# Kernel optimization log

Hardware: AMD Instinct MI355X
Metric: run time of the kernel (lower is better)

The kernel has to match this reference:

```python
import jax, jax.numpy as jnp
import numpy as np

H = 4096      # hidden_size
NH = 32       # num heads
HD = H // NH  # head_dim = 128
I = 11008     # intermediate_size
T = 1024      # prompt tokens
G = 128       # AWQ group size
EPS = 1e-6
ROPE_BASE = 10000.0


def _pack4(key, in_f, out_f):
    # pack 8 uint4 nibbles per int32, [in_f, out_f/8]
    nib = jax.random.randint(key, (in_f, out_f // 8, 8), 0, 16, dtype=jnp.int32)
    shifts = (jnp.arange(8, dtype=jnp.int32) * 4)
    return jnp.bitwise_or.reduce(nib << shifts, axis=-1).astype(jnp.int32)


def _dequant(qw, qz, sc):
    # qw:[in,out/8] int32, qz:[in/G,out/8] int32, sc:[in/G,out] float
    shifts = jnp.arange(8, dtype=jnp.int32) * 4
    w = ((qw[:, :, None] >> shifts) & 0xF).reshape(qw.shape[0], -1)   # [in,out]
    z = ((qz[:, :, None] >> shifts) & 0xF).reshape(qz.shape[0], -1)   # [groups,out]
    gidx = jnp.arange(qw.shape[0]) // G
    return (w.astype(sc.dtype) - z.astype(sc.dtype)[gidx]) * sc[gidx]


def _qlinear(x, qw, qz, sc):
    return x @ _dequant(qw, qz, sc)


def _rmsnorm(x, w):
    var = jnp.mean(x * x, axis=-1, keepdims=True)
    return x * jax.lax.rsqrt(var + EPS) * w


def _rope(x, positions):
    # x: [T, NH, HD], neox-style half rotation (vLLM rotary)
    inv = 1.0 / (ROPE_BASE ** (jnp.arange(0, HD, 2, dtype=jnp.float32) / HD))
    freqs = positions.astype(jnp.float32)[:, None] * inv[None, :]     # [T, HD/2]
    cos = jnp.cos(freqs)[:, None, :]
    sin = jnp.sin(freqs)[:, None, :]
    x1, x2 = jnp.split(x, 2, axis=-1)
    return jnp.concatenate([x1 * cos - x2 * sin, x2 * cos + x1 * sin], axis=-1)


def _attention(positions, q, k, v):
    # causal self-attention over the prompt (prefill writes k/v to cache then attends)
    q = _rope(q.reshape(T, NH, HD), positions)
    k = _rope(k.reshape(T, NH, HD), positions)
    v = v.reshape(T, NH, HD)
    scale = HD ** -0.5
    scores = jnp.einsum('qhd,khd->hqk', q, k) * scale
    mask = jnp.tril(jnp.ones((T, T), dtype=bool))
    scores = jnp.where(mask[None], scores, jnp.finfo(scores.dtype).min)
    probs = jax.nn.softmax(scores, axis=-1)
    out = jnp.einsum('hqk,khd->qhd', probs, v)
    return out.reshape(T, NH * HD)


def setup_inputs() -> dict:
    key = jax.random.key(0)
    ks = jax.random.split(key, 16)
    S = 0.002  # AWQ scale magnitude
    inp = {
        'positions': jnp.arange(T, dtype=jnp.int32),
        'hidden_states': jax.random.normal(ks[0], (T, H), dtype=jnp.float32),
        'ln1_w': jnp.ones((H,), dtype=jnp.float32),
        'ln2_w': jnp.ones((H,), dtype=jnp.float32),
        'qkv_qw': _pack4(ks[1], H, 3 * H),
        'qkv_qz': _pack4(ks[2], H // G, 3 * H),
        'qkv_sc': jax.random.uniform(ks[3], (H // G, 3 * H), dtype=jnp.float32) * S,
        'o_qw': _pack4(ks[4], H, H),
        'o_qz': _pack4(ks[5], H // G, H),
        'o_sc': jax.random.uniform(ks[6], (H // G, H), dtype=jnp.float32) * S,
        'gate_qw': _pack4(ks[7], H, I),
        'gate_qz': _pack4(ks[8], H // G, I),
        'gate_sc': jax.random.uniform(ks[9], (H // G, I), dtype=jnp.float32) * S,
        'up_qw': _pack4(ks[10], H, I),
        'up_qz': _pack4(ks[11], H // G, I),
        'up_sc': jax.random.uniform(ks[12], (H // G, I), dtype=jnp.float32) * S,
        'down_qw': _pack4(ks[13], I, H),
        'down_qz': _pack4(ks[14], I // G, H),
        'down_sc': jax.random.uniform(ks[15], (I // G, H), dtype=jnp.float32) * S,
    }
    return inp


def reference(positions, hidden_states, ln1_w, qkv_qw, qkv_qz, qkv_sc,
              o_qw, o_qz, o_sc, gate_qw, gate_qz, gate_sc,
              up_qw, up_qz, up_sc, down_qw, down_qz, down_sc, ln2_w):
    # --- self attention block ---
    residual = hidden_states
    x = _rmsnorm(hidden_states, ln1_w)
    qkv = _qlinear(x, qkv_qw, qkv_qz, qkv_sc)                # [T, 3H]
    q, k, v = jnp.split(qkv, 3, axis=-1)
    attn_out = _attention(positions, q, k, v)                # [T, H]
    x = _qlinear(attn_out, o_qw, o_qz, o_sc)
    hidden = residual + x
    # --- MLP block ---
    residual = hidden
    x = _rmsnorm(hidden, ln2_w)
    gate = jax.nn.silu(_qlinear(x, gate_qw, gate_qz, gate_sc))
    up = _qlinear(x, up_qw, up_qz, up_sc)
    x = _qlinear(gate * up, down_qw, down_qz, down_sc)
    return residual + x
```

## Files before the change

### kernel.cpp

```cpp
#include <hip/hip_runtime.h>
#include <cstdint>

typedef __attribute__((ext_vector_type(8))) short  bf16x8;
typedef __attribute__((ext_vector_type(4))) float  f32x4;
typedef __attribute__((ext_vector_type(4))) unsigned int uint4v;
typedef __attribute__((ext_vector_type(2))) unsigned int uint2v;

typedef const __attribute__((address_space(1))) void* gas_t;
typedef __attribute__((address_space(3))) void* las_t;

__device__ __forceinline__ float bf2f(unsigned short b) {
    union { unsigned int u; float f; } v; v.u = ((unsigned int)b) << 16; return v.f;
}
__device__ __forceinline__ unsigned short f2bf(float f) {
    union { float f; unsigned int u; } v; v.f = f;
    unsigned int r = v.u + 0x7FFFu + ((v.u >> 16) & 1u);
    return (unsigned short)(r >> 16);
}
__device__ __forceinline__ float u2f(unsigned int u) {
    union { unsigned int u; float f; } v; v.u = u; return v.f;
}

__global__ __launch_bounds__(256)
void dequant_kernel(const int* __restrict__ qw, const int* __restrict__ qz,
                    const float* __restrict__ sc, unsigned short* __restrict__ out,
                    int NW, int K)
{
    const int t   = threadIdx.x;
    const int wcb = blockIdx.x << 5;
    const int kb  = blockIdx.y << 6;
    const int g   = blockIdx.y >> 1;
    const int N   = NW << 3;
    const int wc  = wcb + (t >> 3);
    const int k0  = kb + ((t & 7) << 3);

    unsigned int w[8];
#pragma unroll
    for (int j = 0; j < 8; j++) w[j] = (unsigned int)qw[(size_t)(k0 + j) * NW + wc];
    const unsigned int zw = (unsigned int)qz[(size_t)g * NW + wc];
    float scv[8];
#pragma unroll
    for (int j2 = 0; j2 < 8; j2++) scv[j2] = sc[(size_t)g * N + (wc << 3) + j2];

#pragma unroll
    for (int j2 = 0; j2 < 8; j2++) {
        const int sh = j2 << 2;
        const float s = scv[j2];
        const float moff = -(8388608.0f + (float)((zw >> sh) & 0xFu)) * s;
        unsigned int pk[4];
#pragma unroll
        for (int i = 0; i < 4; i++) {
            float f0 = fmaf(u2f(((w[2*i]   >> sh) & 0xFu) | 0x4B000000u), s, moff);
            float f1 = fmaf(u2f(((w[2*i+1] >> sh) & 0xFu) | 0x4B000000u), s, moff);
            asm("v_cvt_pk_bf16_f32 %0, %1, %2" : "=v"(pk[i]) : "v"(f0), "v"(f1));
        }
        uint4v ov = {pk[0], pk[1], pk[2], pk[3]};
        *(uint4v*)(out + (size_t)((wc << 3) + j2) * K + k0) = ov;
    }
}

__global__ __launch_bounds__(256)
void rmsnorm_kernel(const float* __restrict__ x, const float* __restrict__ wgt,
                    unsigned short* __restrict__ out)
{
    const int t = blockIdx.x, tid = threadIdx.x;
    const float4* xr = (const float4*)(x + (size_t)t * 4096);
    float4 v[4];
    float ss = 0.f;
#pragma unroll
    for (int j = 0; j < 4; j++) {
        v[j] = xr[(j << 8) + tid];
        ss += v[j].x*v[j].x + v[j].y*v[j].y + v[j].z*v[j].z + v[j].w*v[j].w;
    }
#pragma unroll
    for (int m = 1; m < 64; m <<= 1) ss += __shfl_xor(ss, m);
    __shared__ float red[4];
    if ((tid & 63) == 0) red[tid >> 6] = ss;
    __syncthreads();
    float tot = red[0] + red[1] + red[2] + red[3];
    float rs = rsqrtf(tot * (1.f / 4096.f) + 1e-6f);
    const float4* wr = (const float4*)wgt;
#pragma unroll
    for (int j = 0; j < 4; j++) {
        float4 wv = wr[(j << 8) + tid];
        float4 xv = v[j];
        unsigned int p0 = (unsigned int)f2bf(xv.x*rs*wv.x) | ((unsigned int)f2bf(xv.y*rs*wv.y) << 16);
        unsigned int p1 = (unsigned int)f2bf(xv.z*rs*wv.z) | ((unsigned int)f2bf(xv.w*rs*wv.w) << 16);
        uint2v pk = {p0, p1};
        *(uint2v*)(&out[(size_t)t*4096 + (size_t)(((j << 8) + tid) << 2)]) = pk;
    }
}

template<int MODE>
__global__ __launch_bounds__(256, 3)
void bt_gemm(const unsigned short* __restrict__ A,
             const unsigned short* __restrict__ Bt0,
             const unsigned short* __restrict__ Bt1,
             void* __restrict__ out0, void* __restrict__ out1,
             const float* __restrict__ res,
             int N, int K)
{
    __shared__ unsigned short As[128 * 64];
    __shared__ unsigned short Bs[128 * 64];

    const int tid  = threadIdx.x;
    const int lane = tid & 63;
    const int wid  = tid >> 6;
    const int wm   = wid >> 1, wn = wid & 1;
    const int m0   = blockIdx.y << 7;
    const int n0   = blockIdx.x << 7;

    const unsigned short* Bt = Bt0;
    void* outp = out0;
    if (MODE == 1 && blockIdx.z == 1) { Bt = Bt1; outp = out1; }

    f32x4 acc[4][4];
#pragma unroll
    for (int i = 0; i < 4; i++)
#pragma unroll
        for (int j = 0; j < 4; j++) { f32x4 zv = {0.f,0.f,0.f,0.f}; acc[i][j] = zv; }

    const int nsteps = K >> 6;
    for (int t = 0; t < nsteps; t++) {
        const int k0 = t << 6;
        __syncthreads();
#pragma unroll
        for (int i = 0; i < 4; i++) {
            int slot = (i << 8) + tid;
            int row = slot >> 3, s = slot & 7;
            __builtin_amdgcn_global_load_lds(
                (gas_t)(A + (size_t)(m0 + row) * K + k0 + ((s ^ (row & 7)) << 3)),
                (las_t)&As[slot << 3], 16, 0, 0);
        }
#pragma unroll
        for (int i = 0; i < 4; i++) {
            int slot = (i << 8) + tid;
            int row = slot >> 3, s = slot & 7;
            __builtin_amdgcn_global_load_lds(
                (gas_t)(Bt + (size_t)(n0 + row) * K + k0 + ((s ^ (row & 7)) << 3)),
                (las_t)&Bs[slot << 3], 16, 0, 0);
        }
        __syncthreads();
#pragma unroll
        for (int kk = 0; kk < 2; kk++) {
            const int srow = (kk << 2) + (lane >> 4);
            bf16x8 af[4], bfv[4];
#pragma unroll
            for (int mi = 0; mi < 4; mi++) {
                int r = (wm << 6) + (mi << 4) + (lane & 15);
                af[mi] = *(const bf16x8*)(&As[(r << 6) + ((srow ^ (r & 7)) << 3)]);
            }
#pragma unroll
            for (int ni = 0; ni < 4; ni++) {
                int r = (wn << 6) + (ni << 4) + (lane & 15);
                bfv[ni] = *(const bf16x8*)(&Bs[(r << 6) + ((srow ^ (r & 7)) << 3)]);
            }
#pragma unroll
            for (int mi = 0; mi < 4; mi++)
#pragma unroll
                for (int ni = 0; ni < 4; ni++)
                    acc[mi][ni] = __builtin_amdgcn_mfma_f32_16x16x32_bf16(af[mi], bfv[ni], acc[mi][ni], 0, 0, 0);
        }
    }

    const int rbase = m0 + (wm << 6) + ((lane >> 4) << 2);
    const int cbase = n0 + (wn << 6) + (lane & 15);
#pragma unroll
    for (int mi = 0; mi < 4; mi++) {
#pragma unroll
        for (int r = 0; r < 4; r++) {
            int row = rbase + (mi << 4) + r;
#pragma unroll
            for (int ni = 0; ni < 4; ni++) {
                int col = cbase + (ni << 4);
                float v = acc[mi][ni][r];
                if (MODE == 3) {
                    ((float*)out0)[(size_t)row * N + col] = v + res[(size_t)row * N + col];
                } else {
                    ((unsigned short*)outp)[(size_t)row * N + col] = f2bf(v);
                }
            }
        }
    }
}

__global__ __launch_bounds__(256)
void rope_kernel(const int* __restrict__ positions, const unsigned short* __restrict__ qkv,
                 unsigned short* __restrict__ Qr, unsigned short* __restrict__ Kr,
                 unsigned short* __restrict__ Vtp)
{
    const int t = blockIdx.x, tid = threadIdx.x;
    const float p = (float)positions[t];
    const unsigned short* row = qkv + (size_t)t * 12288;
#pragma unroll 4
    for (int it = 0; it < 16; it++) {
        int task = (it << 8) + tid;
        int i   = task & 63;
        int hh  = (task >> 6) & 31;
        int isK = task >> 11;
        float fr = p * __expf(-(float)i * 0.14391156831f);
        float s, c;
        __sincosf(fr, &s, &c);
        const unsigned short* src = row + (isK << 12) + (hh << 7);
        float x1 = bf2f(src[i]);
        float x2 = bf2f(src[64 + i]);
        float o1 = x1 * c - x2 * s;
        float o2 = x2 * c + x1 * s;
        if (!isK) { o1 *= 0.08838834764831845f; o2 *= 0.08838834764831845f; }
        unsigned short* dst = (isK ? Kr : Qr) + ((size_t)hh * 1024 + t) * 128;
        dst[i]      = f2bf(o1);
        dst[64 + i] = f2bf(o2);
    }
#pragma unroll 4
    for (int it = 0; it < 16; it++) {
        int task = (it << 8) + tid;
        int d = task & 127, hh = task >> 7;
        Vtp[((size_t)hh * 128 + d) * 1024 + t] = row[8192 + task];
    }
}

__global__ __launch_bounds__(256, 2)
void attn_kernel(const unsigned short* __restrict__ Qr, const unsigned short* __restrict__ Kr,
                 const unsigned short* __restrict__ Vtp, unsigned short* __restrict__ attn_out)
{
    __shared__ unsigned short Ks[64 * 128];
    __shared__ unsigned short Vs[128 * 64];
    __shared__ unsigned short Ps[4][16 * 64];
    const int tid = threadIdx.x, lane = tid & 63, w = tid >> 6;
    const int qt = blockIdx.x, h = blockIdx.y;

    const unsigned short* Qh = Qr + ((size_t)h * 1024 + (size_t)qt * 64) * 128;

    bf16x8 qf[4];
#pragma unroll
    for (int kk = 0; kk < 4; kk++)
        qf[kk] = *(const bf16x8*)(Qh + (size_t)((w << 4) + (lane & 15)) * 128 + (kk << 5) + ((lane >> 4) << 3));

    f32x4 o[8];
#pragma unroll
    for (int i = 0; i < 8; i++) { f32x4 zf = {0.f,0.f,0.f,0.f}; o[i] = zf; }
    float Mr[4] = {-1e30f, -1e30f, -1e30f, -1e30f};
    float Lr[4] = {0.f, 0.f, 0.f, 0.f};
    const int qrow0 = (qt << 6) + (w << 4) + ((lane >> 4) << 2);

    for (int kt = 0; kt <= qt; kt++) {
        __syncthreads();
#pragma unroll
        for (int j = 0; j < 4; j++) {
            int slot = (j << 8) + tid;
            int rw = slot >> 4, s = slot & 15;
            int ssrc = (s & 8) | ((s ^ (rw & 7)) & 7);
            const uint4v* src = (const uint4v*)(Kr + ((size_t)h * 1024 + (size_t)kt * 64 + rw) * 128 + (ssrc << 3));
            *(uint4v*)(&Ks[(rw << 7) + (s << 3)]) = *src;
        }
#pragma unroll
        for (int j = 0; j < 4; j++) {
            int slot = (j << 8) + tid;
            int rw = slot >> 3, s = slot & 7;
            const uint4v* src = (const uint4v*)(Vtp + ((size_t)h * 128 + rw) * 1024 + (kt << 6) + ((s ^ (rw & 7)) << 3));
            *(uint4v*)(&Vs[(rw << 6) + (s << 3)]) = *src;
        }
        __syncthreads();

        f32x4 sc4[4];
#pragma unroll
        for (int ni = 0; ni < 4; ni++) { f32x4 zf = {0.f,0.f,0.f,0.f}; sc4[ni] = zf; }
#pragma unroll
        for (int kk = 0; kk < 4; kk++) {
#pragma unroll
            for (int ni = 0; ni < 4; ni++) {
                int r = (ni << 4) + (lane & 15);
                int s = (kk << 2) + (lane >> 4);
                int sp = (s & 8) | ((s ^ (r & 7)) & 7);
                bf16x8 kf = *(const bf16x8*)(&Ks[(r << 7) + (sp << 3)]);
                sc4[ni] = __builtin_amdgcn_mfma_f32_16x16x32_bf16(qf[kk], kf, sc4[ni], 0, 0, 0);
            }
        }

#pragma unroll
        for (int r = 0; r < 4; r++) {
            int qg = qrow0 + r;
            float mx = -1e30f;
#pragma unroll
            for (int ni = 0; ni < 4; ni++) {
                int kg_ = (kt << 6) + (ni << 4) + (lane & 15);
                float v = sc4[ni][r];
                if (kt == qt && kg_ > qg) { v = -1e30f; sc4[ni][r] = v; }
                mx = fmaxf(mx, v);
            }
#pragma unroll
            for (int m_ = 1; m_ < 16; m_ <<= 1) mx = fmaxf(mx, __shfl_xor(mx, m_));
            float mnew  = fmaxf(Mr[r], mx);
            float alpha = __expf(Mr[r] - mnew);
            Mr[r] = mnew;
            float rs = 0.f;
#pragma unroll
            for (int ni = 0; ni < 4; ni++) {
                float pv = __expf(sc4[ni][r] - mnew);
                sc4[ni][r] = pv;
                rs += pv;
            }
#pragma unroll
            for (int m_ = 1; m_ < 16; m_ <<= 1) rs += __shfl_xor(rs, m_);
            Lr[r] = Lr[r] * alpha + rs;
#pragma unroll
            for (int nd = 0; nd < 8; nd++) o[nd][r] *= alpha;
        }

#pragma unroll
        for (int r = 0; r < 4; r++) {
            int qr = ((lane >> 4) << 2) + r;
#pragma unroll
            for (int ni = 0; ni < 4; ni++) {
                int col = (ni << 4) + (lane & 15);
                int phys = (col >> 3) ^ (qr & 7);
                Ps[w][(qr << 6) + (phys << 3) + (col & 7)] = f2bf(sc4[ni][r]);
            }
        }
#pragma unroll
        for (int kk2 = 0; kk2 < 2; kk2++) {
            int rowp = lane & 15;
            int sl = (kk2 << 2) + (lane >> 4);
            bf16x8 pa = *(const bf16x8*)(&Ps[w][(rowp << 6) + ((sl ^ (rowp & 7)) << 3)]);
#pragma unroll
            for (int nd = 0; nd < 8; nd++) {
                int rv = (nd << 4) + (lane & 15);
                bf16x8 vb = *(const bf16x8*)(&Vs[(rv << 6) + ((sl ^ (rv & 7)) << 3)]);
                o[nd] = __builtin_amdgcn_mfma_f32_16x16x32_bf16(pa, vb, o[nd], 0, 0, 0);
            }
        }
    }

#pragma unroll
    for (int r = 0; r < 4; r++) {
        float inv = 1.0f / Lr[r];
        int trow = qrow0 + r;
#pragma unroll
        for (int nd = 0; nd < 8; nd++) {
            int col = (h << 7) + (nd << 4) + (lane & 15);
            attn_out[(size_t)trow * 4096 + col] = f2bf(o[nd][r] * inv);
        }
    }
}

__global__ __launch_bounds__(256)
void silu_mul_kernel(const unsigned short* __restrict__ gate, unsigned short* __restrict__ up)
{
    size_t idx = ((size_t)blockIdx.x * 256 + threadIdx.x) * 8;
    uint4v g = *(const uint4v*)(gate + idx);
    uint4v u = *(const uint4v*)(up + idx);
    unsigned int outp[4];
#pragma unroll
    for (int j = 0; j < 4; j++) {
        unsigned int gw = g[j], uw = u[j];
        float g0 = bf2f((unsigned short)(gw & 0xFFFF)), g1 = bf2f((unsigned short)(gw >> 16));
        float u0 = bf2f((unsigned short)(uw & 0xFFFF)), u1 = bf2f((unsigned short)(uw >> 16));
        float s0 = g0 / (1.f + __expf(-g0)) * u0;
        float s1 = g1 / (1.f + __expf(-g1)) * u1;
        outp[j] = (unsigned int)f2bf(s0) | ((unsigned int)f2bf(s1) << 16);
    }
    uint4v ov = {outp[0], outp[1], outp[2], outp[3]};
    *(uint4v*)(up + idx) = ov;
}

extern "C" void kernel_launch(void* const* d_in, const int* in_sizes, int n_in,
                              void* d_out, int out_size, void* d_ws, size_t ws_size,
                              hipStream_t stream)
{
    const int*   positions = (const int*)  d_in[0];
    const float* hidden    = (const float*)d_in[1];
    const float* ln1       = (const float*)d_in[2];
    const float* ln2       = (const float*)d_in[3];
    const int*   qkv_qw    = (const int*)  d_in[4];
    const int*   qkv_qz    = (const int*)  d_in[5];
    const float* qkv_sc    = (const float*)d_in[6];
    const int*   o_qw      = (const int*)  d_in[7];
    const int*   o_qz      = (const int*)  d_in[8];
    const float* o_sc      = (const float*)d_in[9];
    const int*   gate_qw   = (const int*)  d_in[10];
    const int*   gate_qz   = (const int*)  d_in[11];
    const float* gate_sc   = (const float*)d_in[12];
    const int*   up_qw     = (const int*)  d_in[13];
    const int*   up_qz     = (const int*)  d_in[14];
    const float* up_sc     = (const float*)d_in[15];
    const int*   down_qw   = (const int*)  d_in[16];
    const int*   down_qz   = (const int*)  d_in[17];
    const float* down_sc   = (const float*)d_in[18];

    char* ws = (char*)d_ws;
    const size_t MB = 1 << 20;
    unsigned short* Wt    = (unsigned short*)(ws + 0);
    unsigned short* Wu    = (unsigned short*)(ws + 86 * MB);
    unsigned short* xln   = (unsigned short*)(ws + 176 * MB);
    unsigned short* qkvb  = (unsigned short*)(ws + 184 * MB);
    unsigned short* Qrp   = (unsigned short*)(ws + 208 * MB);
    unsigned short* Krp   = (unsigned short*)(ws + 216 * MB);
    unsigned short* Vtp   = (unsigned short*)(ws + 224 * MB);
    unsigned short* attnb = (unsigned short*)(ws + 232 * MB);
    float*          hid   = (float*)        (ws + 240 * MB);
    unsigned short* x2    = xln;
    unsigned short* gateb = qkvb;
    unsigned short* upb   = Qrp;

    dequant_kernel<<<dim3(48, 64), 256, 0, stream>>>(qkv_qw, qkv_qz, qkv_sc, Wt, 1536, 4096);
    rmsnorm_kernel<<<1024, 256, 0, stream>>>(hidden, ln1, xln);
    bt_gemm<0><<<dim3(96, 8), 256, 0, stream>>>(xln, Wt, nullptr,
                                                (void*)qkvb, nullptr, nullptr, 12288, 4096);
    rope_kernel<<<1024, 256, 0, stream>>>(positions, qkvb, Qrp, Krp, Vtp);
    dequant_kernel<<<dim3(16, 64), 256, 0, stream>>>(o_qw, o_qz, o_sc, Wt, 512, 4096);
    attn_kernel<<<dim3(16, 32), 256, 0, stream>>>(Qrp, Krp, Vtp, attnb);
    bt_gemm<3><<<dim3(32, 8), 256, 0, stream>>>(attnb, Wt, nullptr,
                                                (void*)hid, nullptr, hidden, 4096, 4096);
    rmsnorm_kernel<<<1024, 256, 0, stream>>>(hid, ln2, x2);
    dequant_kernel<<<dim3(43, 64), 256, 0, stream>>>(gate_qw, gate_qz, gate_sc, Wt, 1376, 4096);
    dequant_kernel<<<dim3(43, 64), 256, 0, stream>>>(up_qw, up_qz, up_sc, Wu, 1376, 4096);
    bt_gemm<1><<<dim3(86, 8, 2), 256, 0, stream>>>(x2, Wt, Wu,
                                                   (void*)gateb, (void*)upb, nullptr, 11008, 4096);
    silu_mul_kernel<<<5504, 256, 0, stream>>>(gateb, upb);
    dequant_kernel<<<dim3(16, 172), 256, 0, stream>>>(down_qw, down_qz, down_sc, Wt, 512, 11008);
    bt_gemm<3><<<dim3(32, 8), 256, 0, stream>>>(upb, Wt, nullptr,
                                                d_out, nullptr, hid, 4096, 11008);
}
```

Before: 801.9 us.

## Fuse SiLU-mul into gate GEMM epilogue and swizzle GEMM block order

Removes the separate silu_mul kernel by computing the up projection first and applying SiLU(gate)*up in the gate GEMM's epilogue, which reads the up tile from global memory. The gate/up dual launch is split into two sequential GEMMs. GEMM blocks now use a 1D grid remapped into groups of 8 N-tiles across the 8 M-tiles for L2 reuse. Launch bounds rise from 3 to 4 blocks per SIMD, which may force register spills.

```diff
diff --git a/kernel.cpp b/kernel.cpp
--- a/kernel.cpp
+++ b/kernel.cpp
@@ -92,14 +92,18 @@
 }
 
 template<int MODE>
-__global__ __launch_bounds__(256, 3)
+__global__ __launch_bounds__(256, 4)
 void bt_gemm(const unsigned short* __restrict__ A,
-             const unsigned short* __restrict__ Bt0,
-             const unsigned short* __restrict__ Bt1,
-             void* __restrict__ out0, void* __restrict__ out1,
-             const float* __restrict__ res,
-             int N, int K)
-{
+             const unsigned short* __restrict__ Bt,
+             void* __restrict__ out0, const void* __restrict__ aux,
+             int N, int K, int NB)
+{
+    const int flat = blockIdx.x;
+    const int nb   = (((flat >> 6) << 3)) + (flat & 7);
+    if (nb >= NB) return;
+    const int m0 = ((flat >> 3) & 7) << 7;
+    const int n0 = nb << 7;
+
     __shared__ unsigned short As[128 * 64];
     __shared__ unsigned short Bs[128 * 64];
 
@@ -107,12 +111,6 @@
     const int lane = tid & 63;
     const int wid  = tid >> 6;
     const int wm   = wid >> 1, wn = wid & 1;
-    const int m0   = blockIdx.y << 7;
-    const int n0   = blockIdx.x << 7;
-
-    const unsigned short* Bt = Bt0;
-    void* outp = out0;
-    if (MODE == 1 && blockIdx.z == 1) { Bt = Bt1; outp = out1; }
 
     f32x4 acc[4][4];
 #pragma unroll
@@ -175,9 +173,14 @@
                 int col = cbase + (ni << 4);
                 float v = acc[mi][ni][r];
                 if (MODE == 3) {
-                    ((float*)out0)[(size_t)row * N + col] = v + res[(size_t)row * N + col];
+                    ((float*)out0)[(size_t)row * N + col] =
+                        v + ((const float*)aux)[(size_t)row * N + col];
+                } else if (MODE == 4) {
+                    float u = bf2f(((const unsigned short*)aux)[(size_t)row * N + col]);
+                    float sv = v / (1.f + __expf(-v)) * u;
+                    ((unsigned short*)out0)[(size_t)row * N + col] = f2bf(sv);
                 } else {
-                    ((unsigned short*)outp)[(size_t)row * N + col] = f2bf(v);
+                    ((unsigned short*)out0)[(size_t)row * N + col] = f2bf(v);
                 }
             }
         }
@@ -343,26 +346,6 @@
     }
 }
 
-__global__ __launch_bounds__(256)
-void silu_mul_kernel(const unsigned short* __restrict__ gate, unsigned short* __restrict__ up)
-{
-    size_t idx = ((size_t)blockIdx.x * 256 + threadIdx.x) * 8;
-    uint4v g = *(const uint4v*)(gate + idx);
-    uint4v u = *(const uint4v*)(up + idx);
-    unsigned int outp[4];
-#pragma unroll
-    for (int j = 0; j < 4; j++) {
-        unsigned int gw = g[j], uw = u[j];
-        float g0 = bf2f((unsigned short)(gw & 0xFFFF)), g1 = bf2f((unsigned short)(gw >> 16));
-        float u0 = bf2f((unsigned short)(uw & 0xFFFF)), u1 = bf2f((unsigned short)(uw >> 16));
-        float s0 = g0 / (1.f + __expf(-g0)) * u0;
-        float s1 = g1 / (1.f + __expf(-g1)) * u1;
-        outp[j] = (unsigned int)f2bf(s0) | ((unsigned int)f2bf(s1) << 16);
-    }
-    uint4v ov = {outp[0], outp[1], outp[2], outp[3]};
-    *(uint4v*)(up + idx) = ov;
-}
-
 extern "C" void kernel_launch(void* const* d_in, const int* in_sizes, int n_in,
                               void* d_out, int out_size, void* d_ws, size_t ws_size,
                               hipStream_t stream)
@@ -404,20 +387,16 @@
 
     dequant_kernel<<<dim3(48, 64), 256, 0, stream>>>(qkv_qw, qkv_qz, qkv_sc, Wt, 1536, 4096);
     rmsnorm_kernel<<<1024, 256, 0, stream>>>(hidden, ln1, xln);
-    bt_gemm<0><<<dim3(96, 8), 256, 0, stream>>>(xln, Wt, nullptr,
-                                                (void*)qkvb, nullptr, nullptr, 12288, 4096);
+    bt_gemm<0><<<768, 256, 0, stream>>>(xln, Wt, (void*)qkvb, nullptr, 12288, 4096, 96);
     rope_kernel<<<1024, 256, 0, stream>>>(positions, qkvb, Qrp, Krp, Vtp);
     dequant_kernel<<<dim3(16, 64), 256, 0, stream>>>(o_qw, o_qz, o_sc, Wt, 512, 4096);
     attn_kernel<<<dim3(16, 32), 256, 0, stream>>>(Qrp, Krp, Vtp, attnb);
-    bt_gemm<3><<<dim3(32, 8), 256, 0, stream>>>(attnb, Wt, nullptr,
-                                                (void*)hid, nullptr, hidden, 4096, 4096);
+    bt_gemm<3><<<256, 256, 0, stream>>>(attnb, Wt, (void*)hid, hidden, 4096, 4096, 32);
     rmsnorm_kernel<<<1024, 256, 0, stream>>>(hid, ln2, x2);
+    dequant_kernel<<<dim3(43, 64), 256, 0, stream>>>(up_qw, up_qz, up_sc, Wu, 1376, 4096);
+    bt_gemm<0><<<704, 256, 0, stream>>>(x2, Wu, (void*)upb, nullptr, 11008, 4096, 86);
     dequant_kernel<<<dim3(43, 64), 256, 0, stream>>>(gate_qw, gate_qz, gate_sc, Wt, 1376, 4096);
-    dequant_kernel<<<dim3(43, 64), 256, 0, stream>>>(up_qw, up_qz, up_sc, Wu, 1376, 4096);
-    bt_gemm<1><<<dim3(86, 8, 2), 256, 0, stream>>>(x2, Wt, Wu,
-                                                   (void*)gateb, (void*)upb, nullptr, 11008, 4096);
-    silu_mul_kernel<<<5504, 256, 0, stream>>>(gateb, upb);
+    bt_gemm<4><<<704, 256, 0, stream>>>(x2, Wt, (void*)gateb, upb, 11008, 4096, 86);
     dequant_kernel<<<dim3(16, 172), 256, 0, stream>>>(down_qw, down_qz, down_sc, Wt, 512, 11008);
-    bt_gemm<3><<<dim3(32, 8), 256, 0, stream>>>(upb, Wt, nullptr,
-                                                d_out, nullptr, hid, 4096, 11008);
-}
+    bt_gemm<3><<<256, 256, 0, stream>>>(gateb, Wt, d_out, hid, 4096, 11008, 32);
+}
```

Result: faster. 741.3 us (-7.6%).
